# Optimization experiments

Measured on AMD Instinct MI355X. Metric: run time of the kernel, lower is better.

The kernel has to match this reference:

```python
import jax, jax.numpy as jnp
import numpy as np

N_EMBD = 1024
QK_DIM = 16


def setup_inputs() -> dict:
    key = jax.random.key(0)
    k1, k2, k3, k4, k5 = jax.random.split(key, 5)
    b, s = 8, 2048
    lim = 1.0 / np.sqrt(N_EMBD)  # torch Linear default init range
    return {
        "x": jax.random.normal(k1, (b, s, N_EMBD), dtype=jnp.float32),
        "w_q": jax.random.uniform(k2, (QK_DIM, N_EMBD), minval=-lim, maxval=lim, dtype=jnp.float32),
        "b_q": jax.random.uniform(k3, (QK_DIM,), minval=-lim, maxval=lim, dtype=jnp.float32),
        "w_k": jax.random.uniform(k4, (QK_DIM, N_EMBD), minval=-lim, maxval=lim, dtype=jnp.float32),
        "b_k": jax.random.uniform(k5, (QK_DIM,), minval=-lim, maxval=lim, dtype=jnp.float32),
    }


def reference(x, w_q, b_q, w_k, b_k):
    # x: [b, s, d_model]
    s = x.shape[-2]
    q = jnp.einsum("bsd,ed->bse", x, w_q) + b_q  # [b, s, qk_dim]
    k = jnp.einsum("bsd,ed->bse", x, w_k) + b_k  # [b, s, qk_dim]
    scale = 1.0 / jnp.sqrt(jnp.asarray(QK_DIM, dtype=x.dtype))
    mask = jnp.arange(s)[:, None] >= jnp.arange(s)[None, :]  # causal [s, s]
    scores = jnp.einsum("bqe,bke->bqk", q, k) * scale  # [b, s, s]
    scores = jnp.where(mask[None], scores, jnp.asarray(-10000.0, dtype=x.dtype))
    probs = jax.nn.softmax(scores, axis=-1)
    return jnp.einsum("bqk,bkv->bqv", probs, x)  # identity OV: weighted sum of x
```

## Files before the change

### kernel.cpp

```cpp
#include <hip/hip_runtime.h>

typedef __attribute__((ext_vector_type(4))) float  f32x4;
typedef __attribute__((ext_vector_type(8))) short  bf16x8;
typedef __attribute__((ext_vector_type(4))) unsigned int u32x4;

#define MFMA16(a,b,c) __builtin_amdgcn_mfma_f32_16x16x32_bf16(a,b,c,0,0,0)
#define SCL   0.360673760f
#define PBIAS 17.3123405f

static __device__ __forceinline__ unsigned short f2bf(float f){
  unsigned int u = __float_as_uint(f);
  u += 0x7fffu + ((u>>16)&1u);
  return (unsigned short)(u>>16);
}
static __device__ __forceinline__ unsigned int pk2(float a, float b){
  return (unsigned)f2bf(a) | (((unsigned)f2bf(b))<<16);
}

__global__ __launch_bounds__(256,2) void prep_kernel(
    const float* __restrict__ x,  const float* __restrict__ wq, const float* __restrict__ bq,
    const float* __restrict__ wk, const float* __restrict__ bk,
    unsigned short* __restrict__ qws, unsigned short* __restrict__ kws,
    unsigned char* __restrict__ xpk)
{
  __shared__ __align__(16) unsigned short wlds[32*1032];
  __shared__ __align__(16) unsigned short xlds[64*72];
  const int t  = threadIdx.x;
  const int r0 = blockIdx.x<<6;
  const int b  = r0>>11;
  const int s0 = r0&2047;
  const int l = t&63, w = t>>6, g = l>>4, li = l&15;

  { const int n = t>>3, part = t&7;
    const float* wsrc = (n<16) ? (wq + n*1024) : (wk + (n-16)*1024);
    #pragma unroll
    for(int cc=0; cc<16; ++cc){
      const int d = part*128 + cc*8;
      f32x4 f0 = *(const f32x4*)(wsrc + d);
      f32x4 f1 = *(const f32x4*)(wsrc + d + 4);
      u32x4 p;
      p[0]=pk2(f0[0],f0[1]); p[1]=pk2(f0[2],f0[3]);
      p[2]=pk2(f1[0],f1[1]); p[3]=pk2(f1[2],f1[3]);
      *(u32x4*)(&wlds[n*1032 + d]) = p;
    }
  }
  __syncthreads();

  f32x4 acc0 = {0.f,0.f,0.f,0.f};
  f32x4 acc1 = {0.f,0.f,0.f,0.f};
  const int srow = t>>2, dch = t&3;
  const int dd = t&63, sch = t>>6;

  unsigned char* pdst = xpk + ((size_t)(b*64 + (s0>>5) + (sch>>1)))*65536
                      + (size_t)(dd>>4)*1024 + (size_t)(sch&1)*512 + (size_t)(dd&15)*16;

  for(int it=0; it<16; ++it){
    { const float* xp = x + (size_t)(r0+srow)*1024 + it*64 + dch*16;
      f32x4 a0 = *(const f32x4*)(xp);
      f32x4 a1 = *(const f32x4*)(xp+4);
      f32x4 a2 = *(const f32x4*)(xp+8);
      f32x4 a3 = *(const f32x4*)(xp+12);
      u32x4 p0, p1;
      p0[0]=pk2(a0[0],a0[1]); p0[1]=pk2(a0[2],a0[3]);
      p0[2]=pk2(a1[0],a1[1]); p0[3]=pk2(a1[2],a1[3]);
      p1[0]=pk2(a2[0],a2[1]); p1[1]=pk2(a2[2],a2[3]);
      p1[2]=pk2(a3[0],a3[1]); p1[3]=pk2(a3[2],a3[3]);
      *(u32x4*)(&xlds[srow*72 + dch*16])     = p0;
      *(u32x4*)(&xlds[srow*72 + dch*16 + 8]) = p1;
    }
    __syncthreads();
    #pragma unroll
    for(int ks=0; ks<2; ++ks){
      bf16x8 a  = *(const bf16x8*)(&xlds[(16*w+li)*72       + ks*32 + g*8]);
      bf16x8 b0 = *(const bf16x8*)(&wlds[ li*1032     + it*64 + ks*32 + g*8]);
      bf16x8 b1 = *(const bf16x8*)(&wlds[(16+li)*1032 + it*64 + ks*32 + g*8]);
      acc0 = MFMA16(a,b0,acc0);
      acc1 = MFMA16(a,b1,acc1);
    }
    {
      unsigned short v[16];
      #pragma unroll
      for(int jj=0; jj<16; ++jj) v[jj] = xlds[(sch*16 + jj)*72 + dd];
      u32x4 o0, o1;
      o0[0]=(unsigned)v[0]|((unsigned)v[1]<<16);   o0[1]=(unsigned)v[2]|((unsigned)v[3]<<16);
      o0[2]=(unsigned)v[4]|((unsigned)v[5]<<16);   o0[3]=(unsigned)v[6]|((unsigned)v[7]<<16);
      o1[0]=(unsigned)v[8]|((unsigned)v[9]<<16);   o1[1]=(unsigned)v[10]|((unsigned)v[11]<<16);
      o1[2]=(unsigned)v[12]|((unsigned)v[13]<<16); o1[3]=(unsigned)v[14]|((unsigned)v[15]<<16);
      unsigned char* dst = pdst + (size_t)it*4096;
      *(u32x4*)(dst)       = o0;
      *(u32x4*)(dst + 256) = o1;
    }
    __syncthreads();
  }
  #pragma unroll
  for(int reg=0; reg<4; ++reg){
    const int sr = r0 + 16*w + 4*g + reg;
    qws[(size_t)sr*16 + li] = f2bf(acc0[reg] + bq[li]);
    kws[(size_t)sr*16 + li] = f2bf(acc1[reg] + bk[li]);
  }
}

__global__ __launch_bounds__(256,3) void attn_kernel(
    const unsigned short* __restrict__ qws, const unsigned short* __restrict__ kws,
    const unsigned char* __restrict__ xpk, float* __restrict__ out)
{
  __shared__ __align__(16) unsigned char pshare[8192];
  __shared__ float psL[64];
  const int t = threadIdx.x;
  const int l = t&63, w = t>>6, g = l>>4, li = l&15;
  const int bi = blockIdx.x;
  const int b = bi&7;
  const int j = bi>>3;
  const int qb = 31-(j>>2), dq = j&3;
  const int q0 = qb<<6, d0 = dq<<8, nt = 2*qb + 2;

  const int kperm = ((li>>2)<<3) + (li&3);

  const bf16x8 zero8 = {0,0,0,0,0,0,0,0};
  bf16x8 qfr = zero8;
  if(g < 2) qfr = *(const bf16x8*)(qws + ((size_t)(b*2048 + q0 + 16*w + li)<<4) + 8*g);
  const int qg = q0 + 16*w + li;

  f32x4 acc[4][4];
  #pragma unroll
  for(int i=0;i<4;++i)
    #pragma unroll
    for(int jj=0;jj<4;++jj){ acc[i][jj][0]=0.f; acc[i][jj][1]=0.f; acc[i][jj][2]=0.f; acc[i][jj][3]=0.f; }
  float sp = 0.f;

  const unsigned char* xq = xpk + ((size_t)(b*64)*64 + (size_t)(16*dq + 4*w))*1024 + l*16;
  const unsigned short* kp0 = kws + ((size_t)(b*2048 + kperm)<<4) + 8*g;

  bf16x8 k1 = *(const bf16x8*)(kp0);
  bf16x8 k2 = *(const bf16x8*)(kp0 + 64);
  u32x4 xc[4];
  #pragma unroll
  for(int df=0; df<4; ++df) xc[df] = *(const u32x4*)(xq + df*1024);

  int buf = 0;
  for(int tt=0; tt<nt; ++tt){
    const int kv0 = tt<<5;
    const int tn = (tt+1 < nt) ? tt+1 : tt;
    u32x4 xn[4];
    #pragma unroll
    for(int df=0; df<4; ++df) xn[df] = *(const u32x4*)(xq + (size_t)tn*65536 + df*1024);
    f32x4 z = {0.f,0.f,0.f,0.f};
    f32x4 s1 = MFMA16(k1, qfr, z);
    f32x4 s2 = MFMA16(k2, qfr, z);
    const unsigned short* kpn = kp0 + (size_t)(tn<<5)*16;
    bf16x8 n1 = *(const bf16x8*)(kpn);
    bf16x8 n2 = *(const bf16x8*)(kpn + 64);
    float p[8];
    if(tt < nt-2){
      #pragma unroll
      for(int r=0;r<4;++r){
        p[r]   = exp2f(fmaf(s1[r], SCL, -PBIAS));
        p[4+r] = exp2f(fmaf(s2[r], SCL, -PBIAS));
      }
    } else {
      #pragma unroll
      for(int r=0;r<4;++r){
        p[r]   = (kv0 + 8*g + r   <= qg) ? exp2f(fmaf(s1[r], SCL, -PBIAS)) : 0.f;
        p[4+r] = (kv0 + 8*g + 4+r <= qg) ? exp2f(fmaf(s2[r], SCL, -PBIAS)) : 0.f;
      }
    }
    sp += ((p[0]+p[1])+(p[2]+p[3])) + ((p[4]+p[5])+(p[6]+p[7]));
    { u32x4 av;
      asm("v_cvt_pk_bf16_f32 %0, %1, %2" : "=v"(av[0]) : "v"(p[0]), "v"(p[1]));
      asm("v_cvt_pk_bf16_f32 %0, %1, %2" : "=v"(av[1]) : "v"(p[2]), "v"(p[3]));
      asm("v_cvt_pk_bf16_f32 %0, %1, %2" : "=v"(av[2]) : "v"(p[4]), "v"(p[5]));
      asm("v_cvt_pk_bf16_f32 %0, %1, %2" : "=v"(av[3]) : "v"(p[6]), "v"(p[7]));
      *(u32x4*)(&pshare[buf*4096 + w*1024 + l*16]) = av;
    }
    asm volatile("s_waitcnt lgkmcnt(0)" ::: "memory");
    __builtin_amdgcn_sched_barrier(0);
    __builtin_amdgcn_s_barrier();
    __builtin_amdgcn_sched_barrier(0);
    __builtin_amdgcn_s_setprio(1);
    bf16x8 a0 = *(const bf16x8*)(&pshare[buf*4096 +        l*16]);
    bf16x8 a1 = *(const bf16x8*)(&pshare[buf*4096 + 1024 + l*16]);
    bf16x8 a2 = *(const bf16x8*)(&pshare[buf*4096 + 2048 + l*16]);
    bf16x8 a3 = *(const bf16x8*)(&pshare[buf*4096 + 3072 + l*16]);
    #pragma unroll
    for(int df=0; df<4; ++df){
      bf16x8 bfr = *(const bf16x8*)(&xc[df]);
      acc[0][df] = MFMA16(a0, bfr, acc[0][df]);
      acc[1][df] = MFMA16(a1, bfr, acc[1][df]);
      acc[2][df] = MFMA16(a2, bfr, acc[2][df]);
      acc[3][df] = MFMA16(a3, bfr, acc[3][df]);
    }
    __builtin_amdgcn_s_setprio(0);
    buf ^= 1; k1 = n1; k2 = n2;
    #pragma unroll
    for(int df=0; df<4; ++df) xc[df] = xn[df];
  }

  float r_ = sp;
  r_ += __shfl_xor(r_, 16);
  r_ += __shfl_xor(r_, 32);
  if(l < 16) psL[16*w + l] = r_;
  __syncthreads();
  #pragma unroll
  for(int qf=0; qf<4; ++qf){
    const f32x4 pv = *(const f32x4*)(&psL[16*qf + 4*g]);
    #pragma unroll
    for(int reg=0; reg<4; ++reg){
      const float inv = 1.0f/pv[reg];
      float* op = out + (size_t)(b*2048 + q0 + 16*qf + 4*g + reg)*1024 + d0 + 64*w + li;
      #pragma unroll
      for(int df=0; df<4; ++df) op[df*16] = acc[qf][df][reg]*inv;
    }
  }
}

extern "C" void kernel_launch(void* const* d_in, const int* in_sizes, int n_in,
                              void* d_out, int out_size, void* d_ws, size_t ws_size,
                              hipStream_t stream) {
  (void)in_sizes; (void)n_in; (void)out_size; (void)ws_size;
  const float* x  = (const float*)d_in[0];
  const float* wq = (const float*)d_in[1];
  const float* bq = (const float*)d_in[2];
  const float* wk = (const float*)d_in[3];
  const float* bk = (const float*)d_in[4];
  float* out = (float*)d_out;
  char* ws = (char*)d_ws;
  unsigned short* qws = (unsigned short*)(ws);
  unsigned short* kws = (unsigned short*)(ws + (512<<10));
  unsigned char*  xpk = (unsigned char*)(ws + (2<<20));
  hipLaunchKernelGGL(prep_kernel, dim3(256), dim3(256), 0, stream, x, wq, bq, wk, bk, qws, kws, xpk);
  hipLaunchKernelGGL(attn_kernel, dim3(1024), dim3(256), 0, stream, qws, kws, xpk, out);
}
```

Measured before the change: 73.97 us.

## Double attention block to 512 threads splitting score work across wave halves

The attention kernel now uses 512-thread blocks that each cover 512 output columns instead of 256, so each block reuses one probability tile across twice as many x columns. The score computation for the 32-key tile is split between two wave groups, each doing one MFMA and writing half of the probability row. Per-row sums are combined from both halves before normalisation. The query-block schedule is reordered so the first half of the grid walks from the longest causal rows down and the second half from the shortest up. This halves the redundant score and exp work per output column and changes load balance. In exchange it means fewer, larger blocks and a different occupancy point.

```diff
diff --git a/kernel.cpp b/kernel.cpp
--- a/kernel.cpp
+++ b/kernel.cpp
@@ -3,6 +3,7 @@
 typedef __attribute__((ext_vector_type(4))) float  f32x4;
 typedef __attribute__((ext_vector_type(8))) short  bf16x8;
 typedef __attribute__((ext_vector_type(4))) unsigned int u32x4;
+typedef __attribute__((ext_vector_type(2))) unsigned int u32x2;
 
 #define MFMA16(a,b,c) __builtin_amdgcn_mfma_f32_16x16x32_bf16(a,b,c,0,0,0)
 #define SCL   0.360673760f
@@ -100,26 +101,29 @@
   }
 }
 
-__global__ __launch_bounds__(256,3) void attn_kernel(
+__global__ __launch_bounds__(512,4) void attn_kernel(
     const unsigned short* __restrict__ qws, const unsigned short* __restrict__ kws,
     const unsigned char* __restrict__ xpk, float* __restrict__ out)
 {
   __shared__ __align__(16) unsigned char pshare[8192];
-  __shared__ float psL[64];
+  __shared__ float psL[2][64];
   const int t = threadIdx.x;
   const int l = t&63, w = t>>6, g = l>>4, li = l&15;
+  const int h = w>>2, qf0 = w&3;
   const int bi = blockIdx.x;
   const int b = bi&7;
   const int j = bi>>3;
-  const int qb = 31-(j>>2), dq = j&3;
-  const int q0 = qb<<6, d0 = dq<<8, nt = 2*qb + 2;
+  int qb, dh;
+  if(j < 32){ qb = 31-(j>>1); dh = j&1; }
+  else      { qb = (j-32)>>1; dh = j&1; }
+  const int q0 = qb<<6, d0 = dh<<9, nt = 2*qb + 2;
 
   const int kperm = ((li>>2)<<3) + (li&3);
 
   const bf16x8 zero8 = {0,0,0,0,0,0,0,0};
   bf16x8 qfr = zero8;
-  if(g < 2) qfr = *(const bf16x8*)(qws + ((size_t)(b*2048 + q0 + 16*w + li)<<4) + 8*g);
-  const int qg = q0 + 16*w + li;
+  if(g < 2) qfr = *(const bf16x8*)(qws + ((size_t)(b*2048 + q0 + 16*qf0 + li)<<4) + 8*g);
+  const int qg = q0 + 16*qf0 + li;
 
   f32x4 acc[4][4];
   #pragma unroll
@@ -128,11 +132,10 @@
     for(int jj=0;jj<4;++jj){ acc[i][jj][0]=0.f; acc[i][jj][1]=0.f; acc[i][jj][2]=0.f; acc[i][jj][3]=0.f; }
   float sp = 0.f;
 
-  const unsigned char* xq = xpk + ((size_t)(b*64)*64 + (size_t)(16*dq + 4*w))*1024 + l*16;
-  const unsigned short* kp0 = kws + ((size_t)(b*2048 + kperm)<<4) + 8*g;
-
-  bf16x8 k1 = *(const bf16x8*)(kp0);
-  bf16x8 k2 = *(const bf16x8*)(kp0 + 64);
+  const unsigned char* xq = xpk + (size_t)(b*64)*65536 + (size_t)(32*dh + 4*w)*1024 + l*16;
+  const unsigned short* kp = kws + ((size_t)(b*2048 + kperm)<<4) + 8*g + 64*h;
+
+  bf16x8 k1 = *(const bf16x8*)(kp);
   u32x4 xc[4];
   #pragma unroll
   for(int df=0; df<4; ++df) xc[df] = *(const u32x4*)(xq + df*1024);
@@ -146,31 +149,21 @@
     for(int df=0; df<4; ++df) xn[df] = *(const u32x4*)(xq + (size_t)tn*65536 + df*1024);
     f32x4 z = {0.f,0.f,0.f,0.f};
     f32x4 s1 = MFMA16(k1, qfr, z);
-    f32x4 s2 = MFMA16(k2, qfr, z);
-    const unsigned short* kpn = kp0 + (size_t)(tn<<5)*16;
-    bf16x8 n1 = *(const bf16x8*)(kpn);
-    bf16x8 n2 = *(const bf16x8*)(kpn + 64);
-    float p[8];
+    bf16x8 n1 = *(const bf16x8*)(kp + (size_t)tn*512);
+    float p[4];
     if(tt < nt-2){
       #pragma unroll
-      for(int r=0;r<4;++r){
-        p[r]   = exp2f(fmaf(s1[r], SCL, -PBIAS));
-        p[4+r] = exp2f(fmaf(s2[r], SCL, -PBIAS));
-      }
+      for(int r=0;r<4;++r) p[r] = exp2f(fmaf(s1[r], SCL, -PBIAS));
     } else {
-      #pragma unroll
-      for(int r=0;r<4;++r){
-        p[r]   = (kv0 + 8*g + r   <= qg) ? exp2f(fmaf(s1[r], SCL, -PBIAS)) : 0.f;
-        p[4+r] = (kv0 + 8*g + 4+r <= qg) ? exp2f(fmaf(s2[r], SCL, -PBIAS)) : 0.f;
-      }
-    }
-    sp += ((p[0]+p[1])+(p[2]+p[3])) + ((p[4]+p[5])+(p[6]+p[7]));
-    { u32x4 av;
+      const int kb = kv0 + 8*g + 4*h;
+      #pragma unroll
+      for(int r=0;r<4;++r) p[r] = (kb + r <= qg) ? exp2f(fmaf(s1[r], SCL, -PBIAS)) : 0.f;
+    }
+    sp += (p[0]+p[1])+(p[2]+p[3]);
+    { u32x2 av;
       asm("v_cvt_pk_bf16_f32 %0, %1, %2" : "=v"(av[0]) : "v"(p[0]), "v"(p[1]));
       asm("v_cvt_pk_bf16_f32 %0, %1, %2" : "=v"(av[1]) : "v"(p[2]), "v"(p[3]));
-      asm("v_cvt_pk_bf16_f32 %0, %1, %2" : "=v"(av[2]) : "v"(p[4]), "v"(p[5]));
-      asm("v_cvt_pk_bf16_f32 %0, %1, %2" : "=v"(av[3]) : "v"(p[6]), "v"(p[7]));
-      *(u32x4*)(&pshare[buf*4096 + w*1024 + l*16]) = av;
+      *(u32x2*)(&pshare[buf*4096 + qf0*1024 + l*16 + 8*h]) = av;
     }
     asm volatile("s_waitcnt lgkmcnt(0)" ::: "memory");
     __builtin_amdgcn_sched_barrier(0);
@@ -190,7 +183,7 @@
       acc[3][df] = MFMA16(a3, bfr, acc[3][df]);
     }
     __builtin_amdgcn_s_setprio(0);
-    buf ^= 1; k1 = n1; k2 = n2;
+    buf ^= 1; k1 = n1;
     #pragma unroll
     for(int df=0; df<4; ++df) xc[df] = xn[df];
   }
@@ -198,14 +191,15 @@
   float r_ = sp;
   r_ += __shfl_xor(r_, 16);
   r_ += __shfl_xor(r_, 32);
-  if(l < 16) psL[16*w + l] = r_;
+  if(l < 16) psL[h][16*qf0 + l] = r_;
   __syncthreads();
   #pragma unroll
   for(int qf=0; qf<4; ++qf){
-    const f32x4 pv = *(const f32x4*)(&psL[16*qf + 4*g]);
+    const f32x4 pv0 = *(const f32x4*)(&psL[0][16*qf + 4*g]);
+    const f32x4 pv1 = *(const f32x4*)(&psL[1][16*qf + 4*g]);
     #pragma unroll
     for(int reg=0; reg<4; ++reg){
-      const float inv = 1.0f/pv[reg];
+      const float inv = 1.0f/(pv0[reg] + pv1[reg]);
       float* op = out + (size_t)(b*2048 + q0 + 16*qf + 4*g + reg)*1024 + d0 + 64*w + li;
       #pragma unroll
       for(int df=0; df<4; ++df) op[df*16] = acc[qf][df][reg]*inv;
@@ -228,5 +222,5 @@
   unsigned short* kws = (unsigned short*)(ws + (512<<10));
   unsigned char*  xpk = (unsigned char*)(ws + (2<<20));
   hipLaunchKernelGGL(prep_kernel, dim3(256), dim3(256), 0, stream, x, wq, bq, wk, bk, qws, kws, xpk);
-  hipLaunchKernelGGL(attn_kernel, dim3(1024), dim3(256), 0, stream, qws, kws, xpk, out);
-}
+  hipLaunchKernelGGL(attn_kernel, dim3(512), dim3(512), 0, stream, qws, kws, xpk, out);
+}
```

Result: slower. 135.8 us (+83.6%).
